# Kernel tuning notes

Hardware: AMD Instinct MI355X
Metric: run time of the kernel (lower is better)

## Reference

```python
import jax, jax.numpy as jnp
import numpy as np

# Module config (matches init_kwargs); num_heads must be 1 for the original
# torch code to type-check (score_proj: Linear(d_model, num_heads) applied to
# a head_dim-sized last axis, then squeeze(-1)).
B, S, D, H = 4, 512, 256, 1
DH = D // H  # head_dim == d_model when H == 1


def _linear_init(k, out_f, in_f):
    bound = 1.0 / np.sqrt(in_f)
    kw, kb = jax.random.split(k)
    W = jax.random.uniform(kw, (out_f, in_f), jnp.float32, -bound, bound)
    b = jax.random.uniform(kb, (out_f,), jnp.float32, -bound, bound)
    return W, b


def setup_inputs() -> dict:
    key = jax.random.key(0)
    ks = jax.random.split(key, 8)
    Wq, bq = _linear_init(ks[3], D, D)
    Wk, bk = _linear_init(ks[4], D, D)
    Wv, bv = _linear_init(ks[5], D, D)
    Ws, bs = _linear_init(ks[6], H, D)   # score_proj: d_model -> num_heads
    Wo, bo = _linear_init(ks[7], D, D)
    return {
        "query": jax.random.normal(ks[0], (B, S, D), jnp.float32),
        "key": jax.random.normal(ks[1], (B, S, D), jnp.float32),
        "value": jax.random.normal(ks[2], (B, S, D), jnp.float32),
        "Wq": Wq, "bq": bq, "Wk": Wk, "bk": bk, "Wv": Wv, "bv": bv,
        "Ws": Ws, "bs": bs, "Wo": Wo, "bo": bo,
    }


def reference(query, key, value, Wq, bq, Wk, bk, Wv, bv, Ws, bs, Wo, bo):
    b, s, _ = query.shape
    # Projections, split into heads: (B, H, S, DH)
    q = (query @ Wq.T + bq).reshape(b, s, H, DH).transpose(0, 2, 1, 3)
    k = (key @ Wk.T + bk).reshape(b, s, H, DH).transpose(0, 2, 1, 3)
    v = (value @ Wv.T + bv).reshape(b, s, H, DH).transpose(0, 2, 1, 3)
    # Bahdanau additive scores: tanh of pairwise sum -> (B, H, Sq, Sk, DH)
    t = jnp.tanh(q[:, :, :, None, :] + k[:, :, None, :, :])
    # score_proj (out_features == 1 when H == 1), then squeeze(-1)
    scores = jnp.einsum('bhqkd,od->bhqko', t, Ws) + bs  # (B,H,Sq,Sk,1)
    scores = scores[..., 0]                              # (B,H,Sq,Sk)
    attn = jax.nn.softmax(scores, axis=-1)
    # Weighted sum of values, merge heads back: (B, S, D)
    attended = jnp.einsum('bhqk,bhkd->bqhd', attn, v).reshape(b, s, D)
    out = attended @ Wo.T + bo  # dropout p=0.0 (eval) -> identity
    return out, attn
```

## Files before the change

### kernel.cpp

```cpp
#include <hip/hip_runtime.h>

typedef __attribute__((ext_vector_type(8))) short short8;
typedef __attribute__((ext_vector_type(4))) float f32x4;

constexpr int BATCH = 4;
constexpr int SEQ   = 512;
constexpr int DM    = 256;

#define MFMA(a,b,c) __builtin_amdgcn_mfma_f32_16x16x32_bf16((a),(b),(c),0,0,0)

__device__ __forceinline__ unsigned short bf16h(float x) {
    unsigned u = __float_as_uint(x);
    return (unsigned short)((u + 0x7FFF + ((u >> 16) & 1)) >> 16);
}
__device__ __forceinline__ float bf16f(unsigned short h) {
    return __uint_as_float(((unsigned)h) << 16);
}
__device__ __forceinline__ float exp2x_clamped(float x) {
    x = fminf(5.0f, fmaxf(-5.0f, x));
    return __builtin_amdgcn_exp2f(x * 2.8853900817779268f);
}
__device__ __forceinline__ void cvt8(const float* s, int4& h, int4& l) {
    unsigned hw[8], lw[8];
    #pragma unroll
    for (int j = 0; j < 8; ++j) {
        unsigned short hb = bf16h(s[j]);
        hw[j] = hb;
        lw[j] = bf16h(s[j] - bf16f(hb));
    }
    h.x = (int)(hw[0] | (hw[1] << 16)); h.y = (int)(hw[2] | (hw[3] << 16));
    h.z = (int)(hw[4] | (hw[5] << 16)); h.w = (int)(hw[6] | (hw[7] << 16));
    l.x = (int)(lw[0] | (lw[1] << 16)); l.y = (int)(lw[2] | (lw[3] << 16));
    l.z = (int)(lw[4] | (lw[5] << 16)); l.w = (int)(lw[6] | (lw[7] << 16));
}

__global__ __launch_bounds__(256) void conv_kernel(
    const float* __restrict__ q, const float* __restrict__ k, const float* __restrict__ v,
    const float* __restrict__ Wq, const float* __restrict__ Wk,
    const float* __restrict__ Wv, const float* __restrict__ Wo,
    ushort* qh, ushort* ql, ushort* kh, ushort* kl, ushort* vh, ushort* vl,
    ushort* Wqh, ushort* Wql, ushort* Wkh, ushort* Wkl,
    ushort* Wvh, ushort* Wvl, ushort* Woh, ushort* Wol)
{
    const float* s; ushort* h; ushort* l; int n;
    switch (blockIdx.y) {
        case 0: s = q;  h = qh;  l = ql;  n = 524288; break;
        case 1: s = k;  h = kh;  l = kl;  n = 524288; break;
        case 2: s = v;  h = vh;  l = vl;  n = 524288; break;
        case 3: s = Wq; h = Wqh; l = Wql; n = 65536;  break;
        case 4: s = Wk; h = Wkh; l = Wkl; n = 65536;  break;
        case 5: s = Wv; h = Wvh; l = Wvl; n = 65536;  break;
        default:s = Wo; h = Woh; l = Wol; n = 65536;  break;
    }
    int idx = (blockIdx.x * 256 + threadIdx.x) * 8;
    if (idx >= n) return;
    float4 f0 = *(const float4*)(s + idx);
    float4 f1 = *(const float4*)(s + idx + 4);
    float xs[8] = {f0.x, f0.y, f0.z, f0.w, f1.x, f1.y, f1.z, f1.w};
    int4 ph, pl;
    cvt8(xs, ph, pl);
    *(int4*)&h[idx] = ph;
    *(int4*)&l[idx] = pl;
}

template<int EPI, bool F32A>
__device__ __forceinline__ void mfma_core(
    const ushort* __restrict__ Ah, const ushort* __restrict__ Al,
    const float*  __restrict__ A0, const float*  __restrict__ A1, long ldA,
    const ushort* __restrict__ Bh, const ushort* __restrict__ Bl, long ldB,
    float* __restrict__ C, long ldC, const float* __restrict__ bias,
    ushort* __restrict__ Th, ushort* __restrict__ Tl, long ldT)
{
    __shared__ short lds[16384];
    const int tid = threadIdx.x;
    const int i0 = tid, i1 = tid + 256;
    const int r0 = ((i0 >> 7) << 4) | (i0 & 15), r1 = ((i1 >> 7) << 4) | (i1 & 15);
    const int c0 = ((i0 >> 4) & 7) * 8,          c1 = ((i1 >> 4) & 7) * 8;
    const long a0o = (long)r0 * ldA + c0, a1o = (long)r1 * ldA + c1;
    const long b0o = (long)r0 * ldB + c0, b1o = (long)r1 * ldB + c1;

    int4 rah0, rah1, ral0, ral1, rbh0, rbh1, rbl0, rbl1;
    float4 fa00, fa01, fa10, fa11, fb00, fb01, fb10, fb11;

    auto issue_loads = [&](int it) {
        long off = (long)it * 64;
        if constexpr (F32A) {
            fa00 = *(const float4*)(A0 + a0o + off); fa01 = *(const float4*)(A0 + a0o + off + 4);
            fa10 = *(const float4*)(A0 + a1o + off); fa11 = *(const float4*)(A0 + a1o + off + 4);
            fb00 = *(const float4*)(A1 + a0o + off); fb01 = *(const float4*)(A1 + a0o + off + 4);
            fb10 = *(const float4*)(A1 + a1o + off); fb11 = *(const float4*)(A1 + a1o + off + 4);
        } else {
            rah0 = *(const int4*)(Ah + a0o + off); rah1 = *(const int4*)(Ah + a1o + off);
            ral0 = *(const int4*)(Al + a0o + off); ral1 = *(const int4*)(Al + a1o + off);
        }
        rbh0 = *(const int4*)(Bh + b0o + off); rbh1 = *(const int4*)(Bh + b1o + off);
        rbl0 = *(const int4*)(Bl + b0o + off); rbl1 = *(const int4*)(Bl + b1o + off);
    };
    auto write_lds = [&]() {
        if constexpr (F32A) {
            float s0[8] = {fa00.x + fb00.x, fa00.y + fb00.y, fa00.z + fb00.z, fa00.w + fb00.w,
                           fa01.x + fb01.x, fa01.y + fb01.y, fa01.z + fb01.z, fa01.w + fb01.w};
            int4 h, l2; cvt8(s0, h, l2);
            *(int4*)&lds[i0 * 8] = h; *(int4*)&lds[4096 + i0 * 8] = l2;
            float s1[8] = {fa10.x + fb10.x, fa10.y + fb10.y, fa10.z + fb10.z, fa10.w + fb10.w,
                           fa11.x + fb11.x, fa11.y + fb11.y, fa11.z + fb11.z, fa11.w + fb11.w};
            cvt8(s1, h, l2);
            *(int4*)&lds[i1 * 8] = h; *(int4*)&lds[4096 + i1 * 8] = l2;
        } else {
            *(int4*)&lds[i0 * 8] = rah0;        *(int4*)&lds[i1 * 8] = rah1;
            *(int4*)&lds[4096 + i0 * 8] = ral0; *(int4*)&lds[4096 + i1 * 8] = ral1;
        }
        *(int4*)&lds[8192  + i0 * 8] = rbh0; *(int4*)&lds[8192  + i1 * 8] = rbh1;
        *(int4*)&lds[12288 + i0 * 8] = rbl0; *(int4*)&lds[12288 + i1 * 8] = rbl1;
    };

    const int l = tid & 63, w = tid >> 6;
    const int ms = (w >> 1) * 2, ns = (w & 1) * 2;
    f32x4 acc00 = {0,0,0,0}, acc01 = {0,0,0,0}, acc10 = {0,0,0,0}, acc11 = {0,0,0,0};

    issue_loads(0);
    for (int it = 0; it < 4; ++it) {
        write_lds();
        __syncthreads();
        if (it < 3) issue_loads(it + 1);
        const int lo = l * 8;
        #pragma unroll
        for (int ks = 0; ks < 2; ++ks) {
            short8 a0h = *(const short8*)&lds[((ms    ) * 2 + ks) * 512 + lo];
            short8 a1h = *(const short8*)&lds[((ms + 1) * 2 + ks) * 512 + lo];
            short8 a0l = *(const short8*)&lds[4096 + ((ms    ) * 2 + ks) * 512 + lo];
            short8 a1l = *(const short8*)&lds[4096 + ((ms + 1) * 2 + ks) * 512 + lo];
            short8 b0h = *(const short8*)&lds[8192 + ((ns    ) * 2 + ks) * 512 + lo];
            short8 b1h = *(const short8*)&lds[8192 + ((ns + 1) * 2 + ks) * 512 + lo];
            short8 b0l = *(const short8*)&lds[12288 + ((ns    ) * 2 + ks) * 512 + lo];
            short8 b1l = *(const short8*)&lds[12288 + ((ns + 1) * 2 + ks) * 512 + lo];
            acc00 = MFMA(a0h, b0h, acc00); acc00 = MFMA(a0h, b0l, acc00); acc00 = MFMA(a0l, b0h, acc00);
            acc01 = MFMA(a0h, b1h, acc01); acc01 = MFMA(a0h, b1l, acc01); acc01 = MFMA(a0l, b1h, acc01);
            acc10 = MFMA(a1h, b0h, acc10); acc10 = MFMA(a1h, b0l, acc10); acc10 = MFMA(a1l, b0h, acc10);
            acc11 = MFMA(a1h, b1h, acc11); acc11 = MFMA(a1h, b1l, acc11); acc11 = MFMA(a1l, b1h, acc11);
        }
        __syncthreads();
    }

    auto epi = [&](int i, int j, f32x4 a) {
        const int n  = (ns + j) * 16 + (l & 15);
        const int mb = (ms + i) * 16 + (l >> 4) * 4;
        if constexpr (EPI == 1) {
            float bb = bias[n];
            float x0 = a.x + bb, x1 = a.y + bb, x2 = a.z + bb, x3 = a.w + bb;
            unsigned short h0 = bf16h(x0), h1 = bf16h(x1), h2 = bf16h(x2), h3 = bf16h(x3);
            int2 ph, pl;
            ph.x = (int)(h0 | ((unsigned)h1 << 16));
            ph.y = (int)(h2 | ((unsigned)h3 << 16));
            pl.x = (int)(bf16h(x0 - bf16f(h0)) | ((unsigned)bf16h(x1 - bf16f(h1)) << 16));
            pl.y = (int)(bf16h(x2 - bf16f(h2)) | ((unsigned)bf16h(x3 - bf16f(h3)) << 16));
            *(int2*)&Th[(long)n * ldT + mb] = ph;
            *(int2*)&Tl[(long)n * ldT + mb] = pl;
        } else {
            float bb = (EPI == 2) ? 0.f : bias[n];
            float xs[4] = {a.x, a.y, a.z, a.w};
            #pragma unroll
            for (int r = 0; r < 4; ++r) {
                float x = xs[r] + bb;
                if constexpr (EPI == 0) x = exp2x_clamped(x);
                C[(long)(mb + r) * ldC + n] = x;
            }
        }
    };
    epi(0, 0, acc00); epi(0, 1, acc01); epi(1, 0, acc10); epi(1, 1, acc11);
}

__global__ __launch_bounds__(256) void proj_mfma(
    const ushort* qh, const ushort* ql, const ushort* kh, const ushort* kl,
    const ushort* vh, const ushort* vl,
    const ushort* Wqh, const ushort* Wql, const ushort* Wkh, const ushort* Wkl,
    const ushort* Wvh, const ushort* Wvl,
    const float* bq, const float* bk, const float* bv,
    float* Eq, float* Ek, ushort* vpTh, ushort* vpTl)
{
    const int z = blockIdx.z;
    const long m0 = blockIdx.x * 64, n0 = blockIdx.y * 64;
    const ushort *Ah, *Al, *Bh, *Bl; const float* bias;
    if (z == 0)      { Ah = qh; Al = ql; Bh = Wqh; Bl = Wql; bias = bq; }
    else if (z == 1) { Ah = kh; Al = kl; Bh = Wkh; Bl = Wkl; bias = bk; }
    else             { Ah = vh; Al = vl; Bh = Wvh; Bl = Wvl; bias = bv; }
    Ah += m0 * 256; Al += m0 * 256; Bh += n0 * 256; Bl += n0 * 256; bias += n0;
    if (z < 2) {
        float* C = (z ? Ek : Eq) + m0 * 256 + n0;
        mfma_core<0, false>(Ah, Al, nullptr, nullptr, 256, Bh, Bl, 256,
                            C, 256, bias, nullptr, nullptr, 0);
    } else {
        mfma_core<1, false>(Ah, Al, nullptr, nullptr, 256, Bh, Bl, 256,
                            nullptr, 0, bias,
                            vpTh + n0 * 2048 + m0, vpTl + n0 * 2048 + m0, 2048);
    }
}

__global__ __launch_bounds__(256) void attnv_mfma(
    const ushort* attn_h, const ushort* attn_l,
    const ushort* vpTh, const ushort* vpTl, float* att0, float* att1)
{
    const int z = blockIdx.z, b = z >> 1, h = z & 1;
    const long m0 = blockIdx.x * 64, n0 = blockIdx.y * 64;
    const long arow = (long)b * SEQ + m0;
    const ushort* Ah = attn_h + arow * SEQ + h * 256;
    const ushort* Al = attn_l + arow * SEQ + h * 256;
    const ushort* Bh = vpTh + n0 * 2048 + (long)b * SEQ + h * 256;
    const ushort* Bl = vpTl + n0 * 2048 + (long)b * SEQ + h * 256;
    float* C = (h ? att1 : att0) + arow * DM + n0;
    mfma_core<2, false>(Ah, Al, nullptr, nullptr, SEQ, Bh, Bl, 2048,
                        C, DM, nullptr, nullptr, nullptr, 0);
}

__global__ __launch_bounds__(256) void out_mfma(
    const float* att0, const float* att1,
    const ushort* Woh, const ushort* Wol, const float* bo, float* out)
{
    const long m0 = blockIdx.x * 64, n0 = blockIdx.y * 64;
    mfma_core<3, true>(nullptr, nullptr, att0 + m0 * 256, att1 + m0 * 256, 256,
                       Woh + n0 * 256, Wol + n0 * 256, 256,
                       out + m0 * 256 + n0, 256, bo + n0, nullptr, nullptr, 0);
}

__global__ __launch_bounds__(256) void scores_kernel(
    const float* __restrict__ Eq, const float* __restrict__ Ek,
    const float* __restrict__ Ws, float* __restrict__ part)
{
    __shared__ __align__(16) float qL[64][68];
    __shared__ __align__(16) float kL[64][68];
    const int z = blockIdx.z;
    const int b = z >> 1, c = z & 1;
    const int q0 = blockIdx.x * 64, k0 = blockIdx.y * 64;
    const int tid = threadIdx.x;
    const int qi = tid >> 4, ki = tid & 15;

    float acc[4][4] = {};
    for (int cc = 0; cc < 2; ++cc) {
        const int c0 = c * 128 + cc * 64;
        const float* Eqb = Eq + ((long)b * SEQ + q0) * DM + c0;
        const float* Ekb = Ek + ((long)b * SEQ + k0) * DM + c0;
        if (cc) __syncthreads();
        #pragma unroll
        for (int i = 0; i < 4; ++i) {
            int f = i * 256 + tid;
            int r = f >> 4, col = (f & 15) << 2;
            *(float4*)&qL[r][col] = *(const float4*)(Eqb + (long)r * DM + col);
            *(float4*)&kL[r][col] = *(const float4*)(Ekb + (long)r * DM + col);
        }
        __syncthreads();
        #pragma unroll 2
        for (int d = 0; d < 64; d += 4) {
            float4 w4 = *(const float4*)(Ws + c0 + d);
            float4 av[4], bv[4];
            #pragma unroll
            for (int i = 0; i < 4; ++i) av[i] = *(const float4*)&qL[qi + 16 * i][d];
            #pragma unroll
            for (int j = 0; j < 4; ++j) bv[j] = *(const float4*)&kL[ki + 16 * j][d];
            #pragma unroll
            for (int i = 0; i < 4; ++i)
                #pragma unroll
                for (int j = 0; j < 4; ++j) {
                    float xp = fmaf(av[i].x, bv[j].x, 1.0f);
                    float yp = fmaf(av[i].y, bv[j].y, 1.0f);
                    float zp = fmaf(av[i].z, bv[j].z, 1.0f);
                    float wp = fmaf(av[i].w, bv[j].w, 1.0f);
                    float xy = xp * yp, zw = zp * wp;
                    float n1 = fmaf(w4.x, yp, w4.y * xp);
                    float n2 = fmaf(w4.z, wp, w4.w * zp);
                    float num = fmaf(n1, zw, n2 * xy);
                    acc[i][j] = fmaf(num, __builtin_amdgcn_rcpf(xy * zw), acc[i][j]);
                }
        }
    }

    float* pb = part + (long)c * (BATCH * SEQ * SEQ) + (long)b * SEQ * SEQ;
    #pragma unroll
    for (int i = 0; i < 4; ++i) {
        float* row = pb + (long)(q0 + qi + 16 * i) * SEQ + k0 + ki;
        #pragma unroll
        for (int j = 0; j < 4; ++j) row[16 * j] = acc[i][j];
    }
}

__global__ __launch_bounds__(256) void softmax_kernel(
    const float* __restrict__ part, float* __restrict__ attn,
    ushort* __restrict__ attn_h, ushort* __restrict__ attn_l)
{
    __shared__ float red[8];
    const int tid = threadIdx.x;
    const long row = blockIdx.x;
    constexpr long PS = (long)BATCH * SEQ * SEQ;
    const float* p = part + row * SEQ + tid * 2;
    float2 v0 = *(const float2*)(p);
    float2 v1 = *(const float2*)(p + PS);
    float sx = -2.0f * (v0.x + v1.x);
    float sy = -2.0f * (v0.y + v1.y);

    float m = fmaxf(sx, sy);
    #pragma unroll
    for (int off = 32; off; off >>= 1) m = fmaxf(m, __shfl_xor(m, off));
    int wave = tid >> 6;
    if ((tid & 63) == 0) red[wave] = m;
    __syncthreads();
    m = fmaxf(fmaxf(red[0], red[1]), fmaxf(red[2], red[3]));
    constexpr float L2E = 1.4426950408889634f;
    float e0 = __builtin_amdgcn_exp2f((sx - m) * L2E);
    float e1 = __builtin_amdgcn_exp2f((sy - m) * L2E);
    float s = e0 + e1;
    #pragma unroll
    for (int off = 32; off; off >>= 1) s += __shfl_xor(s, off);
    if ((tid & 63) == 0) red[4 + wave] = s;
    __syncthreads();
    float tot = (red[4] + red[5]) + (red[6] + red[7]);
    float inv = __builtin_amdgcn_rcpf(tot);
    float2 o; o.x = e0 * inv; o.y = e1 * inv;
    *(float2*)(attn + row * SEQ + tid * 2) = o;

    unsigned short h0 = bf16h(o.x), h1 = bf16h(o.y);
    unsigned hp = h0 | ((unsigned)h1 << 16);
    unsigned lp = bf16h(o.x - bf16f(h0)) | ((unsigned)bf16h(o.y - bf16f(h1)) << 16);
    *(unsigned*)&attn_h[row * SEQ + tid * 2] = hp;
    *(unsigned*)&attn_l[row * SEQ + tid * 2] = lp;
}

extern "C" void kernel_launch(void* const* d_in, const int* in_sizes, int n_in,
                              void* d_out, int out_size, void* d_ws, size_t ws_size,
                              hipStream_t stream) {
    const float* query = (const float*)d_in[0];
    const float* key   = (const float*)d_in[1];
    const float* value = (const float*)d_in[2];
    const float* Wq = (const float*)d_in[3];
    const float* bq = (const float*)d_in[4];
    const float* Wk = (const float*)d_in[5];
    const float* bk = (const float*)d_in[6];
    const float* Wv = (const float*)d_in[7];
    const float* bv = (const float*)d_in[8];
    const float* Ws = (const float*)d_in[9];
    const float* Wo = (const float*)d_in[11];
    const float* bo = (const float*)d_in[12];

    float* out  = (float*)d_out;
    float* attn = (float*)d_out + (long)BATCH * SEQ * DM;

    float* ws = (float*)d_ws;
    float* Eq = ws;
    float* Ek = ws + 524288;
    ushort* u = (ushort*)(ws + 1048576);
    ushort* qh  = u;              ushort* ql  = qh  + 524288;
    ushort* kh  = ql  + 524288;   ushort* kl  = kh  + 524288;
    ushort* vh  = kl  + 524288;   ushort* vl  = vh  + 524288;
    ushort* Wqh = vl  + 524288;   ushort* Wql = Wqh + 65536;
    ushort* Wkh = Wql + 65536;    ushort* Wkl = Wkh + 65536;
    ushort* Wvh = Wkl + 65536;    ushort* Wvl = Wvh + 65536;
    ushort* Woh = Wvl + 65536;    ushort* Wol = Woh + 65536;
    ushort* vpTh   = Wol + 65536;    ushort* vpTl   = vpTh + 524288;
    ushort* attn_h = vpTl + 524288;  ushort* attn_l = attn_h + 1048576;
    float* part = (float*)(attn_l + 1048576);
    float* att0 = part;
    float* att1 = part + 524288;

    conv_kernel  <<<dim3(256, 7),   256, 0, stream>>>(query, key, value, Wq, Wk, Wv, Wo,
                                                      qh, ql, kh, kl, vh, vl,
                                                      Wqh, Wql, Wkh, Wkl, Wvh, Wvl, Woh, Wol);
    proj_mfma    <<<dim3(32, 4, 3), 256, 0, stream>>>(qh, ql, kh, kl, vh, vl,
                                                      Wqh, Wql, Wkh, Wkl, Wvh, Wvl,
                                                      bq, bk, bv, Eq, Ek, vpTh, vpTl);
    scores_kernel<<<dim3(8, 8, 8),  256, 0, stream>>>(Eq, Ek, Ws, part);
    softmax_kernel<<<dim3(2048),    256, 0, stream>>>(part, attn, attn_h, attn_l);
    attnv_mfma   <<<dim3(8, 4, 8),  256, 0, stream>>>(attn_h, attn_l, vpTh, vpTl, att0, att1);
    out_mfma     <<<dim3(32, 4),    256, 0, stream>>>(att0, att1, Woh, Wol, bo, out);
}
```

Baseline: 71.65 us.

## Fuse activation bf16 split into projection GEMM and split scores over four chunks

The standalone conversion of query/key/value into hi/lo bf16 buffers is removed, and the projection GEMM now loads fp32 activations and splits them into hi/lo while staging into LDS. Only the four weight matrices are still pre-converted. Separately, the scores kernel splits the head dimension into four 64-wide chunks instead of two, doubling the grid to give more parallelism. Softmax then sums four partial score buffers instead of two. This trades extra partial-buffer traffic and a larger workspace for fewer passes over the activations and better occupancy in the tanh-heavy scores stage.

```diff
diff --git a/kernel.cpp b/kernel.cpp
--- a/kernel.cpp
+++ b/kernel.cpp
@@ -34,26 +34,20 @@
     l.z = (int)(lw[4] | (lw[5] << 16)); l.w = (int)(lw[6] | (lw[7] << 16));
 }
 
-__global__ __launch_bounds__(256) void conv_kernel(
-    const float* __restrict__ q, const float* __restrict__ k, const float* __restrict__ v,
+__global__ __launch_bounds__(256) void conv_w(
     const float* __restrict__ Wq, const float* __restrict__ Wk,
     const float* __restrict__ Wv, const float* __restrict__ Wo,
-    ushort* qh, ushort* ql, ushort* kh, ushort* kl, ushort* vh, ushort* vl,
     ushort* Wqh, ushort* Wql, ushort* Wkh, ushort* Wkl,
     ushort* Wvh, ushort* Wvl, ushort* Woh, ushort* Wol)
 {
-    const float* s; ushort* h; ushort* l; int n;
+    const float* s; ushort* h; ushort* l;
     switch (blockIdx.y) {
-        case 0: s = q;  h = qh;  l = ql;  n = 524288; break;
-        case 1: s = k;  h = kh;  l = kl;  n = 524288; break;
-        case 2: s = v;  h = vh;  l = vl;  n = 524288; break;
-        case 3: s = Wq; h = Wqh; l = Wql; n = 65536;  break;
-        case 4: s = Wk; h = Wkh; l = Wkl; n = 65536;  break;
-        case 5: s = Wv; h = Wvh; l = Wvl; n = 65536;  break;
-        default:s = Wo; h = Woh; l = Wol; n = 65536;  break;
+        case 0: s = Wq; h = Wqh; l = Wql; break;
+        case 1: s = Wk; h = Wkh; l = Wkl; break;
+        case 2: s = Wv; h = Wvh; l = Wvl; break;
+        default:s = Wo; h = Woh; l = Wol; break;
     }
     int idx = (blockIdx.x * 256 + threadIdx.x) * 8;
-    if (idx >= n) return;
     float4 f0 = *(const float4*)(s + idx);
     float4 f1 = *(const float4*)(s + idx + 4);
     float xs[8] = {f0.x, f0.y, f0.z, f0.w, f1.x, f1.y, f1.z, f1.w};
@@ -63,7 +57,7 @@
     *(int4*)&l[idx] = pl;
 }
 
-template<int EPI, bool F32A>
+template<int EPI, int ASRC>
 __device__ __forceinline__ void mfma_core(
     const ushort* __restrict__ Ah, const ushort* __restrict__ Al,
     const float*  __restrict__ A0, const float*  __restrict__ A1, long ldA,
@@ -84,11 +78,13 @@
 
     auto issue_loads = [&](int it) {
         long off = (long)it * 64;
-        if constexpr (F32A) {
+        if constexpr (ASRC != 0) {
             fa00 = *(const float4*)(A0 + a0o + off); fa01 = *(const float4*)(A0 + a0o + off + 4);
             fa10 = *(const float4*)(A0 + a1o + off); fa11 = *(const float4*)(A0 + a1o + off + 4);
-            fb00 = *(const float4*)(A1 + a0o + off); fb01 = *(const float4*)(A1 + a0o + off + 4);
-            fb10 = *(const float4*)(A1 + a1o + off); fb11 = *(const float4*)(A1 + a1o + off + 4);
+            if constexpr (ASRC == 2) {
+                fb00 = *(const float4*)(A1 + a0o + off); fb01 = *(const float4*)(A1 + a0o + off + 4);
+                fb10 = *(const float4*)(A1 + a1o + off); fb11 = *(const float4*)(A1 + a1o + off + 4);
+            }
         } else {
             rah0 = *(const int4*)(Ah + a0o + off); rah1 = *(const int4*)(Ah + a1o + off);
             ral0 = *(const int4*)(Al + a0o + off); ral1 = *(const int4*)(Al + a1o + off);
@@ -97,13 +93,22 @@
         rbl0 = *(const int4*)(Bl + b0o + off); rbl1 = *(const int4*)(Bl + b1o + off);
     };
     auto write_lds = [&]() {
-        if constexpr (F32A) {
-            float s0[8] = {fa00.x + fb00.x, fa00.y + fb00.y, fa00.z + fb00.z, fa00.w + fb00.w,
-                           fa01.x + fb01.x, fa01.y + fb01.y, fa01.z + fb01.z, fa01.w + fb01.w};
-            int4 h, l2; cvt8(s0, h, l2);
+        if constexpr (ASRC != 0) {
+            float s0[8], s1[8];
+            if constexpr (ASRC == 2) {
+                s0[0]=fa00.x+fb00.x; s0[1]=fa00.y+fb00.y; s0[2]=fa00.z+fb00.z; s0[3]=fa00.w+fb00.w;
+                s0[4]=fa01.x+fb01.x; s0[5]=fa01.y+fb01.y; s0[6]=fa01.z+fb01.z; s0[7]=fa01.w+fb01.w;
+                s1[0]=fa10.x+fb10.x; s1[1]=fa10.y+fb10.y; s1[2]=fa10.z+fb10.z; s1[3]=fa10.w+fb10.w;
+                s1[4]=fa11.x+fb11.x; s1[5]=fa11.y+fb11.y; s1[6]=fa11.z+fb11.z; s1[7]=fa11.w+fb11.w;
+            } else {
+                s0[0]=fa00.x; s0[1]=fa00.y; s0[2]=fa00.z; s0[3]=fa00.w;
+                s0[4]=fa01.x; s0[5]=fa01.y; s0[6]=fa01.z; s0[7]=fa01.w;
+                s1[0]=fa10.x; s1[1]=fa10.y; s1[2]=fa10.z; s1[3]=fa10.w;
+                s1[4]=fa11.x; s1[5]=fa11.y; s1[6]=fa11.z; s1[7]=fa11.w;
+            }
+            int4 h, l2;
+            cvt8(s0, h, l2);
             *(int4*)&lds[i0 * 8] = h; *(int4*)&lds[4096 + i0 * 8] = l2;
-            float s1[8] = {fa10.x + fb10.x, fa10.y + fb10.y, fa10.z + fb10.z, fa10.w + fb10.w,
-                           fa11.x + fb11.x, fa11.y + fb11.y, fa11.z + fb11.z, fa11.w + fb11.w};
             cvt8(s1, h, l2);
             *(int4*)&lds[i1 * 8] = h; *(int4*)&lds[4096 + i1 * 8] = l2;
         } else {
@@ -171,8 +176,7 @@
 }
 
 __global__ __launch_bounds__(256) void proj_mfma(
-    const ushort* qh, const ushort* ql, const ushort* kh, const ushort* kl,
-    const ushort* vh, const ushort* vl,
+    const float* __restrict__ q, const float* __restrict__ k, const float* __restrict__ v,
     const ushort* Wqh, const ushort* Wql, const ushort* Wkh, const ushort* Wkl,
     const ushort* Wvh, const ushort* Wvl,
     const float* bq, const float* bk, const float* bv,
@@ -180,19 +184,19 @@
 {
     const int z = blockIdx.z;
     const long m0 = blockIdx.x * 64, n0 = blockIdx.y * 64;
-    const ushort *Ah, *Al, *Bh, *Bl; const float* bias;
-    if (z == 0)      { Ah = qh; Al = ql; Bh = Wqh; Bl = Wql; bias = bq; }
-    else if (z == 1) { Ah = kh; Al = kl; Bh = Wkh; Bl = Wkl; bias = bk; }
-    else             { Ah = vh; Al = vl; Bh = Wvh; Bl = Wvl; bias = bv; }
-    Ah += m0 * 256; Al += m0 * 256; Bh += n0 * 256; Bl += n0 * 256; bias += n0;
+    const float* A; const ushort *Bh, *Bl; const float* bias;
+    if (z == 0)      { A = q; Bh = Wqh; Bl = Wql; bias = bq; }
+    else if (z == 1) { A = k; Bh = Wkh; Bl = Wkl; bias = bk; }
+    else             { A = v; Bh = Wvh; Bl = Wvl; bias = bv; }
+    A += m0 * 256; Bh += n0 * 256; Bl += n0 * 256; bias += n0;
     if (z < 2) {
         float* C = (z ? Ek : Eq) + m0 * 256 + n0;
-        mfma_core<0, false>(Ah, Al, nullptr, nullptr, 256, Bh, Bl, 256,
-                            C, 256, bias, nullptr, nullptr, 0);
+        mfma_core<0, 1>(nullptr, nullptr, A, nullptr, 256, Bh, Bl, 256,
+                        C, 256, bias, nullptr, nullptr, 0);
     } else {
-        mfma_core<1, false>(Ah, Al, nullptr, nullptr, 256, Bh, Bl, 256,
-                            nullptr, 0, bias,
-                            vpTh + n0 * 2048 + m0, vpTl + n0 * 2048 + m0, 2048);
+        mfma_core<1, 1>(nullptr, nullptr, A, nullptr, 256, Bh, Bl, 256,
+                        nullptr, 0, bias,
+                        vpTh + n0 * 2048 + m0, vpTl + n0 * 2048 + m0, 2048);
     }
 }
 
@@ -208,8 +212,8 @@
     const ushort* Bh = vpTh + n0 * 2048 + (long)b * SEQ + h * 256;
     const ushort* Bl = vpTl + n0 * 2048 + (long)b * SEQ + h * 256;
     float* C = (h ? att1 : att0) + arow * DM + n0;
-    mfma_core<2, false>(Ah, Al, nullptr, nullptr, SEQ, Bh, Bl, 2048,
-                        C, DM, nullptr, nullptr, nullptr, 0);
+    mfma_core<2, 0>(Ah, Al, nullptr, nullptr, SEQ, Bh, Bl, 2048,
+                    C, DM, nullptr, nullptr, nullptr, 0);
 }
 
 __global__ __launch_bounds__(256) void out_mfma(
@@ -217,9 +221,9 @@
     const ushort* Woh, const ushort* Wol, const float* bo, float* out)
 {
     const long m0 = blockIdx.x * 64, n0 = blockIdx.y * 64;
-    mfma_core<3, true>(nullptr, nullptr, att0 + m0 * 256, att1 + m0 * 256, 256,
-                       Woh + n0 * 256, Wol + n0 * 256, 256,
-                       out + m0 * 256 + n0, 256, bo + n0, nullptr, nullptr, 0);
+    mfma_core<3, 2>(nullptr, nullptr, att0 + m0 * 256, att1 + m0 * 256, 256,
+                    Woh + n0 * 256, Wol + n0 * 256, 256,
+                    out + m0 * 256 + n0, 256, bo + n0, nullptr, nullptr, 0);
 }
 
 __global__ __launch_bounds__(256) void scores_kernel(
@@ -229,48 +233,46 @@
     __shared__ __align__(16) float qL[64][68];
     __shared__ __align__(16) float kL[64][68];
     const int z = blockIdx.z;
-    const int b = z >> 1, c = z & 1;
+    const int b = z >> 2, c = z & 3;
+    const int c0 = c * 64;
     const int q0 = blockIdx.x * 64, k0 = blockIdx.y * 64;
     const int tid = threadIdx.x;
     const int qi = tid >> 4, ki = tid & 15;
+    const float* Eqb = Eq + ((long)b * SEQ + q0) * DM + c0;
+    const float* Ekb = Ek + ((long)b * SEQ + k0) * DM + c0;
+
+    #pragma unroll
+    for (int i = 0; i < 4; ++i) {
+        int f = i * 256 + tid;
+        int r = f >> 4, col = (f & 15) << 2;
+        *(float4*)&qL[r][col] = *(const float4*)(Eqb + (long)r * DM + col);
+        *(float4*)&kL[r][col] = *(const float4*)(Ekb + (long)r * DM + col);
+    }
+    __syncthreads();
 
     float acc[4][4] = {};
-    for (int cc = 0; cc < 2; ++cc) {
-        const int c0 = c * 128 + cc * 64;
-        const float* Eqb = Eq + ((long)b * SEQ + q0) * DM + c0;
-        const float* Ekb = Ek + ((long)b * SEQ + k0) * DM + c0;
-        if (cc) __syncthreads();
-        #pragma unroll
-        for (int i = 0; i < 4; ++i) {
-            int f = i * 256 + tid;
-            int r = f >> 4, col = (f & 15) << 2;
-            *(float4*)&qL[r][col] = *(const float4*)(Eqb + (long)r * DM + col);
-            *(float4*)&kL[r][col] = *(const float4*)(Ekb + (long)r * DM + col);
-        }
-        __syncthreads();
-        #pragma unroll 2
-        for (int d = 0; d < 64; d += 4) {
-            float4 w4 = *(const float4*)(Ws + c0 + d);
-            float4 av[4], bv[4];
+    #pragma unroll 2
+    for (int d = 0; d < 64; d += 4) {
+        float4 w4 = *(const float4*)(Ws + c0 + d);
+        float4 av[4], bv[4];
+        #pragma unroll
+        for (int i = 0; i < 4; ++i) av[i] = *(const float4*)&qL[qi + 16 * i][d];
+        #pragma unroll
+        for (int j = 0; j < 4; ++j) bv[j] = *(const float4*)&kL[ki + 16 * j][d];
+        #pragma unroll
+        for (int i = 0; i < 4; ++i)
             #pragma unroll
-            for (int i = 0; i < 4; ++i) av[i] = *(const float4*)&qL[qi + 16 * i][d];
-            #pragma unroll
-            for (int j = 0; j < 4; ++j) bv[j] = *(const float4*)&kL[ki + 16 * j][d];
-            #pragma unroll
-            for (int i = 0; i < 4; ++i)
-                #pragma unroll
-                for (int j = 0; j < 4; ++j) {
-                    float xp = fmaf(av[i].x, bv[j].x, 1.0f);
-                    float yp = fmaf(av[i].y, bv[j].y, 1.0f);
-                    float zp = fmaf(av[i].z, bv[j].z, 1.0f);
-                    float wp = fmaf(av[i].w, bv[j].w, 1.0f);
-                    float xy = xp * yp, zw = zp * wp;
-                    float n1 = fmaf(w4.x, yp, w4.y * xp);
-                    float n2 = fmaf(w4.z, wp, w4.w * zp);
-                    float num = fmaf(n1, zw, n2 * xy);
-                    acc[i][j] = fmaf(num, __builtin_amdgcn_rcpf(xy * zw), acc[i][j]);
-                }
-        }
+            for (int j = 0; j < 4; ++j) {
+                float xp = fmaf(av[i].x, bv[j].x, 1.0f);
+                float yp = fmaf(av[i].y, bv[j].y, 1.0f);
+                float zp = fmaf(av[i].z, bv[j].z, 1.0f);
+                float wp = fmaf(av[i].w, bv[j].w, 1.0f);
+                float xy = xp * yp, zw = zp * wp;
+                float n1 = fmaf(w4.x, yp, w4.y * xp);
+                float n2 = fmaf(w4.z, wp, w4.w * zp);
+                float num = fmaf(n1, zw, n2 * xy);
+                acc[i][j] = fmaf(num, __builtin_amdgcn_rcpf(xy * zw), acc[i][j]);
+            }
     }
 
     float* pb = part + (long)c * (BATCH * SEQ * SEQ) + (long)b * SEQ * SEQ;
@@ -293,8 +295,10 @@
     const float* p = part + row * SEQ + tid * 2;
     float2 v0 = *(const float2*)(p);
     float2 v1 = *(const float2*)(p + PS);
-    float sx = -2.0f * (v0.x + v1.x);
-    float sy = -2.0f * (v0.y + v1.y);
+    float2 v2 = *(const float2*)(p + 2 * PS);
+    float2 v3 = *(const float2*)(p + 3 * PS);
+    float sx = -2.0f * ((v0.x + v1.x) + (v2.x + v3.x));
+    float sy = -2.0f * ((v0.y + v1.y) + (v2.y + v3.y));
 
     float m = fmaxf(sx, sy);
     #pragma unroll
@@ -343,29 +347,26 @@
     float* attn = (float*)d_out + (long)BATCH * SEQ * DM;
 
     float* ws = (float*)d_ws;
-    float* Eq = ws;
-    float* Ek = ws + 524288;
-    ushort* u = (ushort*)(ws + 1048576);
-    ushort* qh  = u;              ushort* ql  = qh  + 524288;
-    ushort* kh  = ql  + 524288;   ushort* kl  = kh  + 524288;
-    ushort* vh  = kl  + 524288;   ushort* vl  = vh  + 524288;
-    ushort* Wqh = vl  + 524288;   ushort* Wql = Wqh + 65536;
+    float* Eq   = ws;
+    float* Ek   = ws + 524288;
+    float* part = ws + 1048576;
+    float* att0 = part;
+    float* att1 = part + 524288;
+    ushort* u = (ushort*)(ws + 1048576 + 4194304);
+    ushort* Wqh = u;              ushort* Wql = Wqh + 65536;
     ushort* Wkh = Wql + 65536;    ushort* Wkl = Wkh + 65536;
     ushort* Wvh = Wkl + 65536;    ushort* Wvl = Wvh + 65536;
     ushort* Woh = Wvl + 65536;    ushort* Wol = Woh + 65536;
     ushort* vpTh   = Wol + 65536;    ushort* vpTl   = vpTh + 524288;
     ushort* attn_h = vpTl + 524288;  ushort* attn_l = attn_h + 1048576;
-    float* part = (float*)(attn_l + 1048576);
-    float* att0 = part;
-    float* att1 = part + 524288;
-
-    conv_kernel  <<<dim3(256, 7),   256, 0, stream>>>(query, key, value, Wq, Wk, Wv, Wo,
-                                                      qh, ql, kh, kl, vh, vl,
-                                                      Wqh, Wql, Wkh, Wkl, Wvh, Wvl, Woh, Wol);
-    proj_mfma    <<<dim3(32, 4, 3), 256, 0, stream>>>(qh, ql, kh, kl, vh, vl,
+
+    conv_w       <<<dim3(32, 4),    256, 0, stream>>>(Wq, Wk, Wv, Wo,
+                                                      Wqh, Wql, Wkh, Wkl,
+                                                      Wvh, Wvl, Woh, Wol);
+    proj_mfma    <<<dim3(32, 4, 3), 256, 0, stream>>>(query, key, value,
                                                       Wqh, Wql, Wkh, Wkl, Wvh, Wvl,
                                                       bq, bk, bv, Eq, Ek, vpTh, vpTl);
-    scores_kernel<<<dim3(8, 8, 8),  256, 0, stream>>>(Eq, Ek, Ws, part);
+    scores_kernel<<<dim3(8, 8, 16), 256, 0, stream>>>(Eq, Ek, Ws, part);
     softmax_kernel<<<dim3(2048),    256, 0, stream>>>(part, attn, attn_h, attn_l);
     attnv_mfma   <<<dim3(8, 4, 8),  256, 0, stream>>>(attn_h, attn_l, vpTh, vpTl, att0, att1);
     out_mfma     <<<dim3(32, 4),    256, 0, stream>>>(att0, att1, Woh, Wol, bo, out);
```

After: 72.38 us. No clear change (+1.0%).

## Fuse softmax into attention-times-V MFMA kernel, dropping bf16 attn intermediates

Applied to the files above, without the earlier changes.

Removes the separate softmax kernel. The attn@V kernel now reads the partial scores directly, computes each row's exp-sum up front, and exponentiates tiles on the fly before splitting them into bf16 hi/lo in LDS. Normalization is folded into the epilogue, and only the y==0 blocks write the fp32 attn output. This saves one launch and the write and re-read of the bf16 attn hi/lo buffers. The cost is that exp and row-sum work is repeated across the four n-blocks, and the max-subtraction step is dropped on the assumption that scores are bounded.

```diff
diff --git a/kernel.cpp b/kernel.cpp
--- a/kernel.cpp
+++ b/kernel.cpp
@@ -63,7 +63,7 @@
     *(int4*)&l[idx] = pl;
 }
 
-template<int EPI, bool F32A>
+template<int EPI, int ASRC>
 __device__ __forceinline__ void mfma_core(
     const ushort* __restrict__ Ah, const ushort* __restrict__ Al,
     const float*  __restrict__ A0, const float*  __restrict__ A1, long ldA,
@@ -80,15 +80,15 @@
     const long b0o = (long)r0 * ldB + c0, b1o = (long)r1 * ldB + c1;
 
     int4 rah0, rah1, ral0, ral1, rbh0, rbh1, rbl0, rbl1;
-    float4 fa00, fa01, fa10, fa11, fb00, fb01, fb10, fb11;
+    float4 fa00, fa01, fa10, fa11, ga00, ga01, ga10, ga11;
 
     auto issue_loads = [&](int it) {
         long off = (long)it * 64;
-        if constexpr (F32A) {
+        if constexpr (ASRC == 2) {
             fa00 = *(const float4*)(A0 + a0o + off); fa01 = *(const float4*)(A0 + a0o + off + 4);
             fa10 = *(const float4*)(A0 + a1o + off); fa11 = *(const float4*)(A0 + a1o + off + 4);
-            fb00 = *(const float4*)(A1 + a0o + off); fb01 = *(const float4*)(A1 + a0o + off + 4);
-            fb10 = *(const float4*)(A1 + a1o + off); fb11 = *(const float4*)(A1 + a1o + off + 4);
+            ga00 = *(const float4*)(A1 + a0o + off); ga01 = *(const float4*)(A1 + a0o + off + 4);
+            ga10 = *(const float4*)(A1 + a1o + off); ga11 = *(const float4*)(A1 + a1o + off + 4);
         } else {
             rah0 = *(const int4*)(Ah + a0o + off); rah1 = *(const int4*)(Ah + a1o + off);
             ral0 = *(const int4*)(Al + a0o + off); ral1 = *(const int4*)(Al + a1o + off);
@@ -97,13 +97,14 @@
         rbl0 = *(const int4*)(Bl + b0o + off); rbl1 = *(const int4*)(Bl + b1o + off);
     };
     auto write_lds = [&]() {
-        if constexpr (F32A) {
-            float s0[8] = {fa00.x + fb00.x, fa00.y + fb00.y, fa00.z + fb00.z, fa00.w + fb00.w,
-                           fa01.x + fb01.x, fa01.y + fb01.y, fa01.z + fb01.z, fa01.w + fb01.w};
-            int4 h, l2; cvt8(s0, h, l2);
+        if constexpr (ASRC == 2) {
+            float s0[8] = {fa00.x+ga00.x, fa00.y+ga00.y, fa00.z+ga00.z, fa00.w+ga00.w,
+                           fa01.x+ga01.x, fa01.y+ga01.y, fa01.z+ga01.z, fa01.w+ga01.w};
+            float s1[8] = {fa10.x+ga10.x, fa10.y+ga10.y, fa10.z+ga10.z, fa10.w+ga10.w,
+                           fa11.x+ga11.x, fa11.y+ga11.y, fa11.z+ga11.z, fa11.w+ga11.w};
+            int4 h, l2;
+            cvt8(s0, h, l2);
             *(int4*)&lds[i0 * 8] = h; *(int4*)&lds[4096 + i0 * 8] = l2;
-            float s1[8] = {fa10.x + fb10.x, fa10.y + fb10.y, fa10.z + fb10.z, fa10.w + fb10.w,
-                           fa11.x + fb11.x, fa11.y + fb11.y, fa11.z + fb11.z, fa11.w + fb11.w};
             cvt8(s1, h, l2);
             *(int4*)&lds[i1 * 8] = h; *(int4*)&lds[4096 + i1 * 8] = l2;
         } else {
@@ -157,7 +158,7 @@
             *(int2*)&Th[(long)n * ldT + mb] = ph;
             *(int2*)&Tl[(long)n * ldT + mb] = pl;
         } else {
-            float bb = (EPI == 2) ? 0.f : bias[n];
+            float bb = bias[n];
             float xs[4] = {a.x, a.y, a.z, a.w};
             #pragma unroll
             for (int r = 0; r < 4; ++r) {
@@ -187,39 +188,13 @@
     Ah += m0 * 256; Al += m0 * 256; Bh += n0 * 256; Bl += n0 * 256; bias += n0;
     if (z < 2) {
         float* C = (z ? Ek : Eq) + m0 * 256 + n0;
-        mfma_core<0, false>(Ah, Al, nullptr, nullptr, 256, Bh, Bl, 256,
-                            C, 256, bias, nullptr, nullptr, 0);
+        mfma_core<0, 0>(Ah, Al, nullptr, nullptr, 256, Bh, Bl, 256,
+                        C, 256, bias, nullptr, nullptr, 0);
     } else {
-        mfma_core<1, false>(Ah, Al, nullptr, nullptr, 256, Bh, Bl, 256,
-                            nullptr, 0, bias,
-                            vpTh + n0 * 2048 + m0, vpTl + n0 * 2048 + m0, 2048);
-    }
-}
-
-__global__ __launch_bounds__(256) void attnv_mfma(
-    const ushort* attn_h, const ushort* attn_l,
-    const ushort* vpTh, const ushort* vpTl, float* att0, float* att1)
-{
-    const int z = blockIdx.z, b = z >> 1, h = z & 1;
-    const long m0 = blockIdx.x * 64, n0 = blockIdx.y * 64;
-    const long arow = (long)b * SEQ + m0;
-    const ushort* Ah = attn_h + arow * SEQ + h * 256;
-    const ushort* Al = attn_l + arow * SEQ + h * 256;
-    const ushort* Bh = vpTh + n0 * 2048 + (long)b * SEQ + h * 256;
-    const ushort* Bl = vpTl + n0 * 2048 + (long)b * SEQ + h * 256;
-    float* C = (h ? att1 : att0) + arow * DM + n0;
-    mfma_core<2, false>(Ah, Al, nullptr, nullptr, SEQ, Bh, Bl, 2048,
-                        C, DM, nullptr, nullptr, nullptr, 0);
-}
-
-__global__ __launch_bounds__(256) void out_mfma(
-    const float* att0, const float* att1,
-    const ushort* Woh, const ushort* Wol, const float* bo, float* out)
-{
-    const long m0 = blockIdx.x * 64, n0 = blockIdx.y * 64;
-    mfma_core<3, true>(nullptr, nullptr, att0 + m0 * 256, att1 + m0 * 256, 256,
-                       Woh + n0 * 256, Wol + n0 * 256, 256,
-                       out + m0 * 256 + n0, 256, bo + n0, nullptr, nullptr, 0);
+        mfma_core<1, 0>(Ah, Al, nullptr, nullptr, 256, Bh, Bl, 256,
+                        nullptr, 0, bias,
+                        vpTh + n0 * 2048 + m0, vpTl + n0 * 2048 + m0, 2048);
+    }
 }
 
 __global__ __launch_bounds__(256) void scores_kernel(
@@ -282,45 +257,154 @@
     }
 }
 
-__global__ __launch_bounds__(256) void softmax_kernel(
-    const float* __restrict__ part, float* __restrict__ attn,
-    ushort* __restrict__ attn_h, ushort* __restrict__ attn_l)
-{
-    __shared__ float red[8];
+__global__ __launch_bounds__(256) void attnv_fused(
+    const float* __restrict__ part,
+    const ushort* __restrict__ vpTh, const ushort* __restrict__ vpTl,
+    float* __restrict__ attn, float* __restrict__ att0, float* __restrict__ att1)
+{
+    __shared__ short lds[16384];
+    __shared__ float inv[64];
+    const int z = blockIdx.z, b = z >> 1, h = z & 1;
+    const long m0 = blockIdx.x * 64, n0 = blockIdx.y * 64;
     const int tid = threadIdx.x;
-    const long row = blockIdx.x;
     constexpr long PS = (long)BATCH * SEQ * SEQ;
-    const float* p = part + row * SEQ + tid * 2;
-    float2 v0 = *(const float2*)(p);
-    float2 v1 = *(const float2*)(p + PS);
-    float sx = -2.0f * (v0.x + v1.x);
-    float sy = -2.0f * (v0.y + v1.y);
-
-    float m = fmaxf(sx, sy);
-    #pragma unroll
-    for (int off = 32; off; off >>= 1) m = fmaxf(m, __shfl_xor(m, off));
-    int wave = tid >> 6;
-    if ((tid & 63) == 0) red[wave] = m;
+    constexpr float NL2E = -2.0f * 1.4426950408889634f;
+
+    {
+        const int r = tid >> 2, qn = tid & 3;
+        const float* p0 = part + ((long)b * SEQ + m0 + r) * SEQ + qn * 128;
+        const float* p1 = p0 + PS;
+        float s = 0.f;
+        #pragma unroll 8
+        for (int j = 0; j < 128; j += 4) {
+            float4 a = *(const float4*)(p0 + j);
+            float4 c = *(const float4*)(p1 + j);
+            s += __builtin_amdgcn_exp2f(NL2E * (a.x + c.x));
+            s += __builtin_amdgcn_exp2f(NL2E * (a.y + c.y));
+            s += __builtin_amdgcn_exp2f(NL2E * (a.z + c.z));
+            s += __builtin_amdgcn_exp2f(NL2E * (a.w + c.w));
+        }
+        s += __shfl_xor(s, 1);
+        s += __shfl_xor(s, 2);
+        if (qn == 0) inv[r] = __builtin_amdgcn_rcpf(s);
+    }
     __syncthreads();
-    m = fmaxf(fmaxf(red[0], red[1]), fmaxf(red[2], red[3]));
-    constexpr float L2E = 1.4426950408889634f;
-    float e0 = __builtin_amdgcn_exp2f((sx - m) * L2E);
-    float e1 = __builtin_amdgcn_exp2f((sy - m) * L2E);
-    float s = e0 + e1;
-    #pragma unroll
-    for (int off = 32; off; off >>= 1) s += __shfl_xor(s, off);
-    if ((tid & 63) == 0) red[4 + wave] = s;
-    __syncthreads();
-    float tot = (red[4] + red[5]) + (red[6] + red[7]);
-    float inv = __builtin_amdgcn_rcpf(tot);
-    float2 o; o.x = e0 * inv; o.y = e1 * inv;
-    *(float2*)(attn + row * SEQ + tid * 2) = o;
-
-    unsigned short h0 = bf16h(o.x), h1 = bf16h(o.y);
-    unsigned hp = h0 | ((unsigned)h1 << 16);
-    unsigned lp = bf16h(o.x - bf16f(h0)) | ((unsigned)bf16h(o.y - bf16f(h1)) << 16);
-    *(unsigned*)&attn_h[row * SEQ + tid * 2] = hp;
-    *(unsigned*)&attn_l[row * SEQ + tid * 2] = lp;
+
+    const int i0 = tid, i1 = tid + 256;
+    const int r0 = ((i0 >> 7) << 4) | (i0 & 15), r1 = ((i1 >> 7) << 4) | (i1 & 15);
+    const int c0 = ((i0 >> 4) & 7) * 8,          c1 = ((i1 >> 4) & 7) * 8;
+
+    const ushort* Bh = vpTh + n0 * 2048 + (long)b * SEQ + h * 256;
+    const ushort* Bl = vpTl + n0 * 2048 + (long)b * SEQ + h * 256;
+    const long b0o = (long)r0 * 2048 + c0, b1o = (long)r1 * 2048 + c1;
+
+    const float* pA = part + ((long)b * SEQ + m0) * SEQ + h * 256;
+    float* attnW = (blockIdx.y == 0)
+        ? attn + ((long)b * SEQ + m0) * SEQ + h * 256 : nullptr;
+
+    int4 rbh0, rbh1, rbl0, rbl1;
+    float e0[8], e1[8];
+
+    auto issue = [&](int it) {
+        long off = (long)it * 64;
+        const float* q0p = pA + (long)r0 * SEQ + off + c0;
+        const float* q1p = pA + (long)r1 * SEQ + off + c1;
+        float4 x0 = *(const float4*)(q0p),      x1 = *(const float4*)(q0p + 4);
+        float4 y0 = *(const float4*)(q0p + PS), y1 = *(const float4*)(q0p + PS + 4);
+        float4 u0 = *(const float4*)(q1p),      u1 = *(const float4*)(q1p + 4);
+        float4 v0 = *(const float4*)(q1p + PS), v1 = *(const float4*)(q1p + PS + 4);
+        e0[0] = __builtin_amdgcn_exp2f(NL2E * (x0.x + y0.x));
+        e0[1] = __builtin_amdgcn_exp2f(NL2E * (x0.y + y0.y));
+        e0[2] = __builtin_amdgcn_exp2f(NL2E * (x0.z + y0.z));
+        e0[3] = __builtin_amdgcn_exp2f(NL2E * (x0.w + y0.w));
+        e0[4] = __builtin_amdgcn_exp2f(NL2E * (x1.x + y1.x));
+        e0[5] = __builtin_amdgcn_exp2f(NL2E * (x1.y + y1.y));
+        e0[6] = __builtin_amdgcn_exp2f(NL2E * (x1.z + y1.z));
+        e0[7] = __builtin_amdgcn_exp2f(NL2E * (x1.w + y1.w));
+        e1[0] = __builtin_amdgcn_exp2f(NL2E * (u0.x + v0.x));
+        e1[1] = __builtin_amdgcn_exp2f(NL2E * (u0.y + v0.y));
+        e1[2] = __builtin_amdgcn_exp2f(NL2E * (u0.z + v0.z));
+        e1[3] = __builtin_amdgcn_exp2f(NL2E * (u0.w + v0.w));
+        e1[4] = __builtin_amdgcn_exp2f(NL2E * (u1.x + v1.x));
+        e1[5] = __builtin_amdgcn_exp2f(NL2E * (u1.y + v1.y));
+        e1[6] = __builtin_amdgcn_exp2f(NL2E * (u1.z + v1.z));
+        e1[7] = __builtin_amdgcn_exp2f(NL2E * (u1.w + v1.w));
+        rbh0 = *(const int4*)(Bh + b0o + off); rbh1 = *(const int4*)(Bh + b1o + off);
+        rbl0 = *(const int4*)(Bl + b0o + off); rbl1 = *(const int4*)(Bl + b1o + off);
+    };
+    auto writeL = [&](int it) {
+        int4 hh, ll;
+        cvt8(e0, hh, ll);
+        *(int4*)&lds[i0 * 8] = hh; *(int4*)&lds[4096 + i0 * 8] = ll;
+        cvt8(e1, hh, ll);
+        *(int4*)&lds[i1 * 8] = hh; *(int4*)&lds[4096 + i1 * 8] = ll;
+        *(int4*)&lds[8192  + i0 * 8] = rbh0; *(int4*)&lds[8192  + i1 * 8] = rbh1;
+        *(int4*)&lds[12288 + i0 * 8] = rbl0; *(int4*)&lds[12288 + i1 * 8] = rbl1;
+        if (attnW) {
+            long off = (long)it * 64;
+            float iv0 = inv[r0], iv1 = inv[r1];
+            float* w0 = attnW + (long)r0 * SEQ + off + c0;
+            float* w1 = attnW + (long)r1 * SEQ + off + c1;
+            float4 o;
+            o.x = e0[0]*iv0; o.y = e0[1]*iv0; o.z = e0[2]*iv0; o.w = e0[3]*iv0;
+            *(float4*)w0 = o;
+            o.x = e0[4]*iv0; o.y = e0[5]*iv0; o.z = e0[6]*iv0; o.w = e0[7]*iv0;
+            *(float4*)(w0 + 4) = o;
+            o.x = e1[0]*iv1; o.y = e1[1]*iv1; o.z = e1[2]*iv1; o.w = e1[3]*iv1;
+            *(float4*)w1 = o;
+            o.x = e1[4]*iv1; o.y = e1[5]*iv1; o.z = e1[6]*iv1; o.w = e1[7]*iv1;
+            *(float4*)(w1 + 4) = o;
+        }
+    };
+
+    const int l = tid & 63, w = tid >> 6;
+    const int ms = (w >> 1) * 2, ns = (w & 1) * 2;
+    f32x4 acc00 = {0,0,0,0}, acc01 = {0,0,0,0}, acc10 = {0,0,0,0}, acc11 = {0,0,0,0};
+
+    issue(0);
+    for (int it = 0; it < 4; ++it) {
+        writeL(it);
+        __syncthreads();
+        if (it < 3) issue(it + 1);
+        const int lo = l * 8;
+        #pragma unroll
+        for (int ks = 0; ks < 2; ++ks) {
+            short8 a0h = *(const short8*)&lds[((ms    ) * 2 + ks) * 512 + lo];
+            short8 a1h = *(const short8*)&lds[((ms + 1) * 2 + ks) * 512 + lo];
+            short8 a0l = *(const short8*)&lds[4096 + ((ms    ) * 2 + ks) * 512 + lo];
+            short8 a1l = *(const short8*)&lds[4096 + ((ms + 1) * 2 + ks) * 512 + lo];
+            short8 b0h = *(const short8*)&lds[8192 + ((ns    ) * 2 + ks) * 512 + lo];
+            short8 b1h = *(const short8*)&lds[8192 + ((ns + 1) * 2 + ks) * 512 + lo];
+            short8 b0l = *(const short8*)&lds[12288 + ((ns    ) * 2 + ks) * 512 + lo];
+            short8 b1l = *(const short8*)&lds[12288 + ((ns + 1) * 2 + ks) * 512 + lo];
+            acc00 = MFMA(a0h, b0h, acc00); acc00 = MFMA(a0h, b0l, acc00); acc00 = MFMA(a0l, b0h, acc00);
+            acc01 = MFMA(a0h, b1h, acc01); acc01 = MFMA(a0h, b1l, acc01); acc01 = MFMA(a0l, b1h, acc01);
+            acc10 = MFMA(a1h, b0h, acc10); acc10 = MFMA(a1h, b0l, acc10); acc10 = MFMA(a1l, b0h, acc10);
+            acc11 = MFMA(a1h, b1h, acc11); acc11 = MFMA(a1h, b1l, acc11); acc11 = MFMA(a1l, b1h, acc11);
+        }
+        __syncthreads();
+    }
+
+    float* Cp = (h ? att1 : att0) + ((long)b * SEQ + m0) * DM + n0;
+    auto epi = [&](int i, int j, f32x4 a) {
+        const int n  = (ns + j) * 16 + (l & 15);
+        const int mb = (ms + i) * 16 + (l >> 4) * 4;
+        float xs[4] = {a.x, a.y, a.z, a.w};
+        #pragma unroll
+        for (int r = 0; r < 4; ++r)
+            Cp[(long)(mb + r) * DM + n] = xs[r] * inv[mb + r];
+    };
+    epi(0, 0, acc00); epi(0, 1, acc01); epi(1, 0, acc10); epi(1, 1, acc11);
+}
+
+__global__ __launch_bounds__(256) void out_mfma(
+    const float* att0, const float* att1,
+    const ushort* Woh, const ushort* Wol, const float* bo, float* out)
+{
+    const long m0 = blockIdx.x * 64, n0 = blockIdx.y * 64;
+    mfma_core<2, 2>(nullptr, nullptr, att0 + m0 * 256, att1 + m0 * 256, 256,
+                    Woh + n0 * 256, Wol + n0 * 256, 256,
+                    out + m0 * 256 + n0, 256, bo + n0, nullptr, nullptr, 0);
 }
 
 extern "C" void kernel_launch(void* const* d_in, const int* in_sizes, int n_in,
@@ -343,9 +427,12 @@
     float* attn = (float*)d_out + (long)BATCH * SEQ * DM;
 
     float* ws = (float*)d_ws;
-    float* Eq = ws;
-    float* Ek = ws + 524288;
-    ushort* u = (ushort*)(ws + 1048576);
+    float* Eq   = ws;
+    float* Ek   = ws + 524288;
+    float* part = ws + 1048576;
+    float* att0 = ws + 3145728;
+    float* att1 = ws + 3670016;
+    ushort* u = (ushort*)(ws + 4194304);
     ushort* qh  = u;              ushort* ql  = qh  + 524288;
     ushort* kh  = ql  + 524288;   ushort* kl  = kh  + 524288;
     ushort* vh  = kl  + 524288;   ushort* vl  = vh  + 524288;
@@ -353,11 +440,7 @@
     ushort* Wkh = Wql + 65536;    ushort* Wkl = Wkh + 65536;
     ushort* Wvh = Wkl + 65536;    ushort* Wvl = Wvh + 65536;
     ushort* Woh = Wvl + 65536;    ushort* Wol = Woh + 65536;
-    ushort* vpTh   = Wol + 65536;    ushort* vpTl   = vpTh + 524288;
-    ushort* attn_h = vpTl + 524288;  ushort* attn_l = attn_h + 1048576;
-    float* part = (float*)(attn_l + 1048576);
-    float* att0 = part;
-    float* att1 = part + 524288;
+    ushort* vpTh = Wol + 65536;   ushort* vpTl = vpTh + 524288;
 
     conv_kernel  <<<dim3(256, 7),   256, 0, stream>>>(query, key, value, Wq, Wk, Wv, Wo,
                                                       qh, ql, kh, kl, vh, vl,
@@ -366,7 +449,6 @@
                                                       Wqh, Wql, Wkh, Wkl, Wvh, Wvl,
                                                       bq, bk, bv, Eq, Ek, vpTh, vpTl);
     scores_kernel<<<dim3(8, 8, 8),  256, 0, stream>>>(Eq, Ek, Ws, part);
-    softmax_kernel<<<dim3(2048),    256, 0, stream>>>(part, attn, attn_h, attn_l);
-    attnv_mfma   <<<dim3(8, 4, 8),  256, 0, stream>>>(attn_h, attn_l, vpTh, vpTl, att0, att1);
+    attnv_fused  <<<dim3(8, 4, 8),  256, 0, stream>>>(part, vpTh, vpTl, attn, att0, att1);
     out_mfma     <<<dim3(32, 4),    256, 0, stream>>>(att0, att1, Woh, Wol, bo, out);
 }
```

New measurement: 76.08 us. 1.06x slower.
